# Optimization experiments

Measured on AMD Instinct MI355X. Metric: run time of the kernel, lower is better.

The kernel has to match this reference:

```python
import jax, jax.numpy as jnp
import numpy as np

B, D, H, L, E, NL, P, IMG, NT = 32, 768, 8, 6, 8, 256, 16, 224, 10
G = IMG // P          # 14 patches per side
NP = G * G            # 196 patches
HD = D // H           # 96 head dim
TOPK = 2
KEEP = 0.25
EPS = 1e-5


def layer_norm(x, g, b):
    m = x.mean(-1, keepdims=True)
    v = ((x - m) ** 2).mean(-1, keepdims=True)
    return (x - m) / jnp.sqrt(v + EPS) * g + b


def mha(q, kv, in_w, in_b, out_w, out_b):
    # torch nn.MultiheadAttention: packed in_proj (3D, D), out_proj (D, D)
    wq, wk, wv = in_w[:D], in_w[D:2 * D], in_w[2 * D:]
    bq, bk, bv = in_b[:D], in_b[D:2 * D], in_b[2 * D:]

    def heads(x, w, b):
        y = x @ w.T + b                               # (B, S, D)
        return y.reshape(x.shape[0], x.shape[1], H, HD).transpose(0, 2, 1, 3)

    Q = heads(q, wq, bq)
    K = heads(kv, wk, bk)
    V = heads(kv, wv, bv)
    scores = jnp.einsum('bhqd,bhkd->bhqk', Q, K) / np.sqrt(HD).astype(np.float32)
    attn = jax.nn.softmax(scores, axis=-1)
    o = jnp.einsum('bhqk,bhkd->bhqd', attn, V)
    o = o.transpose(0, 2, 1, 3).reshape(q.shape[0], q.shape[1], D)
    return o @ out_w.T + out_b


def moe(x, rw, rb, w1, b1, w2, b2):
    # top-2 routing; renormalize the top-k weights with a second softmax
    Bq, S, _ = x.shape
    T = Bq * S
    xt = x.reshape(T, D)
    probs = jax.nn.softmax(xt @ rw.T + rb, axis=-1)       # (T, E)
    tw, ti = jax.lax.top_k(probs, TOPK)                   # (T, K)
    tw = jax.nn.softmax(tw, axis=-1)
    # combine weights per expert: (T, E), >0 only for the chosen experts
    combine = (jax.nn.one_hot(ti, E, dtype=x.dtype) * tw[..., None]).sum(axis=1)
    out = jnp.zeros_like(xt)
    for e in range(E):  # fixed small expert count
        h = jax.nn.gelu(xt @ w1[e].T + b1[e], approximate=False)
        out = out + (h @ w2[e].T + b2[e]) * combine[:, e:e + 1]
    return out.reshape(Bq, S, D)


def _forward(images, type_ids, mask_noise, conv_w, conv_b, pos_emb, type_emb,
             latents, ca_in_w, ca_in_b, ca_out_w, ca_out_b, ca_ln_g, ca_ln_b,
             sa_in_w, sa_in_b, sa_out_w, sa_out_b, ln1_g, ln1_b,
             router_w, router_b, e_w1, e_b1, e_w2, e_b2, ln2_g, ln2_b):
    b = images.shape[0]
    # non-overlapping conv patch embed == unfold + matmul
    xp = images.reshape(b, 3, G, P, G, P).transpose(0, 2, 4, 1, 3, 5)
    xp = xp.reshape(b, NP, 3 * P * P)
    patches = xp @ conv_w.reshape(D, -1).T + conv_b        # (B, NP, D)
    patches = patches + pos_emb + type_emb[type_ids][:, None, :]
    # random masking: keep n_visible patches chosen by argsort of noise
    n_visible = int(NP * KEEP)
    order = jnp.argsort(mask_noise, axis=1)
    visible_indices = order[:, :n_visible]
    masked_indices = order[:, n_visible:]
    visible = jnp.take_along_axis(patches, visible_indices[:, :, None], axis=1)
    # cross attention from latents to visible patches
    lat = jnp.broadcast_to(latents, (b, NL, D))
    lat = layer_norm(lat + mha(lat, visible, ca_in_w, ca_in_b, ca_out_w, ca_out_b),
                     ca_ln_g, ca_ln_b)
    for l in range(L):
        a = mha(lat, lat, sa_in_w[l], sa_in_b[l], sa_out_w[l], sa_out_b[l])
        lat = layer_norm(lat + a, ln1_g[l], ln1_b[l])
        m = moe(lat, router_w[l], router_b[l], e_w1[l], e_b1[l], e_w2[l], e_b2[l])
        lat = layer_norm(lat + m, ln2_g[l], ln2_b[l])
    return lat, visible_indices, masked_indices


def setup_inputs() -> dict:
    key = jax.random.key(0)
    ks = jax.random.split(key, 16)
    r = lambda k, shape, s=0.02: jax.random.normal(k, shape, dtype=jnp.float32) * s
    z = lambda shape: jnp.zeros(shape, jnp.float32)
    o = lambda shape: jnp.ones(shape, jnp.float32)
    inp = {}
    inp['images'] = jax.random.normal(ks[0], (B, 3, IMG, IMG), dtype=jnp.float32)
    inp['type_ids'] = jax.random.randint(ks[1], (B,), 0, NT)
    inp['mask_noise'] = jax.random.uniform(ks[2], (B, NP), dtype=jnp.float32)
    inp['conv_w'] = r(ks[3], (D, 3, P, P))
    inp['conv_b'] = z((D,))
    inp['pos_emb'] = r(ks[4], (1, NP, D), 1.0)
    inp['type_emb'] = r(ks[5], (NT, D), 1.0)
    inp['latents'] = r(ks[6], (NL, D), 1.0)
    inp['ca_in_w'] = r(ks[7], (3 * D, D)); inp['ca_in_b'] = z((3 * D,))
    inp['ca_out_w'] = r(ks[8], (D, D)); inp['ca_out_b'] = z((D,))
    inp['ca_ln_g'] = o((D,)); inp['ca_ln_b'] = z((D,))
    inp['sa_in_w'] = r(ks[9], (L, 3 * D, D)); inp['sa_in_b'] = z((L, 3 * D))
    inp['sa_out_w'] = r(ks[10], (L, D, D)); inp['sa_out_b'] = z((L, D))
    inp['ln1_g'] = o((L, D)); inp['ln1_b'] = z((L, D))
    inp['router_w'] = r(ks[11], (L, E, D)); inp['router_b'] = z((L, E))
    inp['e_w1'] = r(ks[12], (L, E, 2 * D, D)); inp['e_b1'] = z((L, E, 2 * D))
    inp['e_w2'] = r(ks[13], (L, E, D, 2 * D)); inp['e_b2'] = z((L, E, D))
    inp['ln2_g'] = o((L, D)); inp['ln2_b'] = z((L, D))
    return inp


def reference(images, type_ids, mask_noise, conv_w, conv_b, pos_emb, type_emb,
              latents, ca_in_w, ca_in_b, ca_out_w, ca_out_b, ca_ln_g, ca_ln_b,
              sa_in_w, sa_in_b, sa_out_w, sa_out_b, ln1_g, ln1_b,
              router_w, router_b, e_w1, e_b1, e_w2, e_b2, ln2_g, ln2_b):
    return _forward(images, type_ids, mask_noise, conv_w, conv_b, pos_emb,
                    type_emb, latents, ca_in_w, ca_in_b, ca_out_w, ca_out_b,
                    ca_ln_g, ca_ln_b, sa_in_w, sa_in_b, sa_out_w, sa_out_b,
                    ln1_g, ln1_b, router_w, router_b, e_w1, e_b1, e_w2, e_b2,
                    ln2_g, ln2_b)
```

## Files before the change

### kernel.cpp

```cpp
#include <hip/hip_runtime.h>

typedef unsigned short u16;
typedef unsigned int u32;
typedef __attribute__((ext_vector_type(8))) u16 u16x8;
typedef __attribute__((ext_vector_type(8))) __bf16 bf16x8;
typedef __attribute__((ext_vector_type(4))) float f32x4;

#define DEV static __device__ __forceinline__

DEV float b2f(u16 u){ unsigned int i = ((unsigned int)u)<<16; float f; __builtin_memcpy(&f,&i,4); return f; }
DEV u16 f2b(float f){ unsigned int x; __builtin_memcpy(&x,&f,4); x = x + 0x7fffu + ((x>>16)&1u); return (u16)(x>>16); }

DEV void gll16(const u16* g, u16* l){
    __builtin_amdgcn_global_load_lds(
        (const __attribute__((address_space(1))) u32*)(const void*)g,
        (__attribute__((address_space(3))) u32*)(void*)l, 16, 0, 0);
}

template<bool F32>
DEV u16x8 ld8(const void* base, long off){
    if constexpr (F32){
        const float* p = (const float*)base + off;
        float4 a = *(const float4*)p;
        float4 b = *(const float4*)(p+4);
        u16x8 r;
        r[0]=f2b(a.x); r[1]=f2b(a.y); r[2]=f2b(a.z); r[3]=f2b(a.w);
        r[4]=f2b(b.x); r[5]=f2b(b.y); r[6]=f2b(b.z); r[7]=f2b(b.w);
        return r;
    } else {
        return *(const u16x8*)((const u16*)base + off);
    }
}
template<bool F32>
DEV const void* vadd(const void* p, long elems){
    if constexpr (F32) return (const void*)((const float*)p + elems);
    else               return (const void*)((const u16*)p + elems);
}

#define LAT_ELEMS 6291456
#define NVIS 49
#define NMASK 147
#define T_TOK 8192
#define MOE_CAP 17408
#define MOE_HALF 8704
#define KOFF 6291456L
#define VOFF 12582912L

__global__ __launch_bounds__(256) void wconv(const float* __restrict__ src, u16* __restrict__ dst, long n)
{
    long i = ((long)blockIdx.x*256 + threadIdx.x)*8;
    if (i >= n) return;
    *(u16x8*)(dst + i) = ld8<true>(src, i);
}

__global__ __launch_bounds__(256) void argsort_k(const float* __restrict__ noise,
                                                 int* __restrict__ order,
                                                 float* __restrict__ dout)
{
    __shared__ float vals[196];
    __shared__ int ord[196];
    int b = blockIdx.x, tid = threadIdx.x;
    if (tid < 196) vals[tid] = noise[b*196 + tid];
    __syncthreads();
    if (tid < 196){
        float vi = vals[tid]; int rank = 0;
        for (int j=0;j<196;j++){ float vj = vals[j]; rank += (vj < vi) || (vj == vi && j < tid); }
        ord[rank] = tid;
    }
    __syncthreads();
    if (tid < 196){
        int v = ord[tid];
        order[b*196 + tid] = v;
        if (tid < NVIS) dout[LAT_ELEMS + b*NVIS + tid] = (float)v;
        else            dout[LAT_ELEMS + 32*NVIS + b*NMASK + (tid - NVIS)] = (float)v;
    }
}

__global__ __launch_bounds__(256) void patch_gather(const float* __restrict__ images,
                                                    const int* __restrict__ order,
                                                    u16* __restrict__ Ap)
{
    int i = blockIdx.x*256 + threadIdx.x;
    int t = i/48, kc = i - t*48;
    if (t >= 1664) return;
    if (t >= 1568){
        u16x8 z{};
        *(u16x8*)(Ap + (long)t*768 + kc*16)     = z;
        *(u16x8*)(Ap + (long)t*768 + kc*16 + 8) = z;
        return;
    }
    int b = t/49, vi = t - b*49;
    int p = order[b*196 + vi];
    int c = kc >> 4, py = kc & 15;
    int gy = p/14, gx = p - gy*14;
    const float* src = images + (((long)(b*3 + c)*224 + gy*16 + py)*224 + gx*16);
    u16x8 o0 = ld8<true>(src, 0);
    u16x8 o1 = ld8<true>(src, 8);
    *(u16x8*)(Ap + (long)t*768 + kc*16)     = o0;
    *(u16x8*)(Ap + (long)t*768 + kc*16 + 8) = o1;
}

__global__ __launch_bounds__(256) void add_pos_type(u16* __restrict__ vis,
                                                    const int* __restrict__ order,
                                                    const int* __restrict__ type_ids,
                                                    const float* __restrict__ pos,
                                                    const float* __restrict__ temb)
{
    int i = blockIdx.x*256 + threadIdx.x;
    int t = i/96, dc = (i - t*96)*8;
    if (t >= 1568) return;
    int b = t/49, vi = t - b*49;
    int p = order[b*196 + vi], tb = type_ids[b];
    u16x8 a = *(u16x8*)(vis + (long)t*768 + dc);
    const float* pp = pos  + (long)p*768 + dc;
    const float* tt = temb + (long)tb*768 + dc;
    float4 p0 = *(const float4*)pp, p1 = *(const float4*)(pp+4);
    float4 t0 = *(const float4*)tt, t1 = *(const float4*)(tt+4);
    u16x8 o;
    o[0]=f2b(b2f(a[0])+p0.x+t0.x); o[1]=f2b(b2f(a[1])+p0.y+t0.y);
    o[2]=f2b(b2f(a[2])+p0.z+t0.z); o[3]=f2b(b2f(a[3])+p0.w+t0.w);
    o[4]=f2b(b2f(a[4])+p1.x+t1.x); o[5]=f2b(b2f(a[5])+p1.y+t1.y);
    o[6]=f2b(b2f(a[6])+p1.z+t1.z); o[7]=f2b(b2f(a[7])+p1.w+t1.w);
    *(u16x8*)(vis + (long)t*768 + dc) = o;
}

template<int BK, bool BIAS, bool GELU, int GRP, bool AF32, bool BF32, bool SWZ, bool GLL>
__global__ __launch_bounds__(256,2) void gemm_nt(
    const void* __restrict__ A, const void* __restrict__ B, const float* __restrict__ bias,
    u16* __restrict__ C,
    int M, int N, int K, int lda, int ldb, int ldc,
    float scale, int ZLO, int NB,
    long sAh, long sAl, long sBh, long sBl, long sCh, long sCl,
    const int* __restrict__ aoff, const int* __restrict__ tos, const u16* __restrict__ zbuf,
    int row_base, long sBE, long sBiasE)
{
    int bx = blockIdx.x, by = blockIdx.y;
    if (SWZ){
        int nx = gridDim.x, ny = gridDim.y;
        int nwg = nx*ny;
        int flat = by*nx + bx;
        int q = nwg >> 3, r = nwg & 7;
        int xcd = flat & 7, idx = flat >> 3;
        int wg = (xcd < r ? xcd*(q+1) : r*(q+1) + (xcd - r)*q) + idx;
        bx = wg % nx; by = wg / nx;
    }
    int z = blockIdx.z; int zh = z / ZLO, zl = z - zh*ZLO;
    const void* Ab = vadd<AF32>(A, zh*sAh + zl*sAl);
    const void* Bb = vadd<BF32>(B, zh*sBh + zl*sBl);
    u16* Cb = C + zh*sCh + zl*sCl;
    const float* biasb = bias;
    int row0 = by*128, col0 = bx*128;
    int lim = 0;
    if (GRP == 1 || GRP == 2){
        lim = aoff[8];
        int g0 = row_base + row0;
        if (g0 >= lim) return;
        int e = 0;
        #pragma unroll
        for (int i=1;i<8;i++) if (g0 >= aoff[i]) e = i;
        Bb = vadd<BF32>(B, (long)e*sBE);
        if (BIAS) biasb = bias + (long)e*sBiasE;
    }
    constexpr int SP = GLL ? BK : BK + 8;
    __shared__ __align__(16) u16 As[128*SP];
    __shared__ __align__(16) u16 Bs[128*SP];
    int tid = threadIdx.x;
    int lane = tid & 63, wv = tid >> 6;
    int wr = (wv>>1)*64, wc = (wv&1)*64;
    f32x4 acc[4][4];
    #pragma unroll
    for (int m=0;m<4;m++){
        #pragma unroll
        for (int n=0;n<4;n++) acc[m][n] = f32x4{0.f,0.f,0.f,0.f};
    }
    constexpr int RPC = BK/8;
    constexpr int PER = 128*RPC/256;
    int tA[4];
    if (GRP == 1){
        if (GLL){
            #pragma unroll
            for (int j=0;j<4;j++){
                int r = wv*32 + j*8 + (lane>>3);
                tA[j] = tos[row_base + row0 + r];
            }
        } else {
            #pragma unroll
            for (int j=0;j<PER && j<4;j++){
                int c = j*256 + tid;
                tA[j] = tos[row_base + row0 + c/RPC];
            }
        }
    }
    for (int k0=0; k0<K; k0+=BK){
        if constexpr (GLL){
            #pragma unroll
            for (int j=0;j<4;j++){
                int r  = wv*32 + j*8 + (lane>>3);
                int ch = lane & 7;
                const u16* sa;
                if (GRP == 1){
                    int t = tA[j];
                    sa = (t >= 0) ? (const u16*)Ab + (long)t*lda + k0 + ch*8 : zbuf + ch*8;
                } else {
                    sa = (const u16*)Ab + (long)(row0+r)*lda + k0 + ch*8;
                }
                gll16(sa, As + (wv*256 + j*64)*8);
                const u16* sb = (const u16*)Bb + (long)(col0+r)*ldb + k0 + ch*8;
                gll16(sb, Bs + (wv*256 + j*64)*8);
            }
        } else {
            #pragma unroll
            for (int j=0;j<PER;j++){
                int c = j*256 + tid;
                int r = c / RPC, cc = (c - r*RPC)*8;
                u16x8 va{}, vb{};
                if (GRP == 1){
                    int t = tA[j];
                    if (t >= 0) va = ld8<AF32>(Ab, (long)t*lda + k0 + cc);
                } else {
                    va = ld8<AF32>(Ab, (long)(row0+r)*lda + k0 + cc);
                }
                if (col0 + r < NB) vb = ld8<BF32>(Bb, (long)(col0+r)*ldb + k0 + cc);
                *(u16x8*)(As + r*SP + cc) = va;
                *(u16x8*)(Bs + r*SP + cc) = vb;
            }
        }
        __syncthreads();
        #pragma unroll
        for (int kk=0; kk<BK/32; kk++){
            bf16x8 af[4], bg[4];
            #pragma unroll
            for (int m=0;m<4;m++)
                af[m] = *(const bf16x8*)(As + (wr + m*16 + (lane&15))*SP + kk*32 + (lane>>4)*8);
            #pragma unroll
            for (int n=0;n<4;n++)
                bg[n] = *(const bf16x8*)(Bs + (wc + n*16 + (lane&15))*SP + kk*32 + (lane>>4)*8);
            #pragma unroll
            for (int m=0;m<4;m++){
                #pragma unroll
                for (int n=0;n<4;n++)
                    acc[m][n] = __builtin_amdgcn_mfma_f32_16x16x32_bf16(af[m], bg[n], acc[m][n], 0,0,0);
            }
        }
        __syncthreads();
    }
    #pragma unroll
    for (int m=0;m<4;m++){
        int rbase = row0 + wr + m*16 + ((lane>>4)<<2);
        #pragma unroll
        for (int n=0;n<4;n++){
            int col = col0 + wc + n*16 + (lane&15);
            if (col < N){
                float bv = BIAS ? biasb[col] : 0.f;
                #pragma unroll
                for (int j=0;j<4;j++){
                    int row = rbase + j;
                    bool ok = (row < M);
                    if (GRP == 1 || GRP == 2) ok = ok && (row_base + row) < lim;
                    if (ok){
                        float v = acc[m][n][j]*scale + bv;
                        if (GELU) v = 0.5f*v*(1.f + erff(v*0.70710678118f));
                        u16 ov = f2b(v);
                        if (GRP == 3){
                            if (col < 768){
                                Cb[(long)row*768 + col] = ov;
                            } else if (col < 1536){
                                Cb[sBE + (long)row*768 + (col - 768)] = ov;
                            } else {
                                int c96 = col - 1536;
                                int h = c96/96, d = c96 - h*96;
                                Cb[sBiasE + ((long)((row>>8)*8 + h)*96 + d)*256 + (row & 255)] = ov;
                            }
                        } else if (GRP == 2){
                            Cb[(long)(row_base + row)*ldc + col] = ov;
                        } else {
                            Cb[(long)row*ldc + col] = ov;
                        }
                    }
                }
            }
        }
    }
}

__global__ __launch_bounds__(256) void ca_attn(const u16* __restrict__ Qc,
                                               const u16* __restrict__ KV,
                                               u16* __restrict__ attn_out)
{
    __shared__ float Sm[256*49];
    __shared__ u16 KVs[49*96];
    int b = blockIdx.x, h = blockIdx.y, q = threadIdx.x;
    for (int i=q; i<49*96; i+=256){ int k=i/96, d=i-k*96; KVs[i] = KV[(long)(b*49+k)*1536 + h*96 + d]; }
    __syncthreads();
    float qv[96];
    #pragma unroll
    for (int d=0;d<96;d++) qv[d] = b2f(Qc[(long)q*768 + h*96 + d]);
    for (int k=0;k<49;k++){
        float a = 0.f;
        #pragma unroll
        for (int d=0;d<96;d++) a += qv[d]*b2f(KVs[k*96+d]);
        Sm[q*49+k] = a*0.10206207f;
    }
    __syncthreads();
    for (int i=q; i<49*96; i+=256){ int k=i/96, d=i-k*96; KVs[i] = KV[(long)(b*49+k)*1536 + 768 + h*96 + d]; }
    float mx = -1e30f;
    for (int k=0;k<49;k++) mx = fmaxf(mx, Sm[q*49+k]);
    float sum = 0.f;
    for (int k=0;k<49;k++){ float e = __expf(Sm[q*49+k]-mx); Sm[q*49+k]=e; sum+=e; }
    float inv = 1.f/sum;
    __syncthreads();
    for (int d=0;d<96;d++){
        float a = 0.f;
        for (int k=0;k<49;k++) a += Sm[q*49+k]*b2f(KVs[k*96+d]);
        attn_out[(long)(b*256+q)*768 + h*96 + d] = f2b(a*inv);
    }
}

__global__ __launch_bounds__(256) void softmax256(u16* __restrict__ S, int rows)
{
    int wid = threadIdx.x >> 6, lane = threadIdx.x & 63;
    int r = blockIdx.x*4 + wid; if (r >= rows) return;
    u16* p = S + (long)r*256;
    ushort4 v = *(const ushort4*)(p + lane*4);
    float x0=b2f(v.x), x1=b2f(v.y), x2=b2f(v.z), x3=b2f(v.w);
    float mx = fmaxf(fmaxf(x0,x1), fmaxf(x2,x3));
    #pragma unroll
    for (int off=32; off>=1; off>>=1) mx = fmaxf(mx, __shfl_xor(mx, off, 64));
    x0=__expf(x0-mx); x1=__expf(x1-mx); x2=__expf(x2-mx); x3=__expf(x3-mx);
    float s = x0+x1+x2+x3;
    #pragma unroll
    for (int off=32; off>=1; off>>=1) s += __shfl_xor(s, off, 64);
    float inv = 1.f/s;
    ushort4 o; o.x=f2b(x0*inv); o.y=f2b(x1*inv); o.z=f2b(x2*inv); o.w=f2b(x3*inv);
    *(ushort4*)(p + lane*4) = o;
}

template<int MODE>
__global__ __launch_bounds__(256) void ln_k(
    const float* __restrict__ res, int resmod,
    const u16* __restrict__ add,
    const u16* __restrict__ OutE, const int* __restrict__ sot, const float2* __restrict__ w01,
    const float* __restrict__ g, const float* __restrict__ bb,
    float* __restrict__ out, u16* __restrict__ outb, int T)
{
    int wid = threadIdx.x >> 6, lane = threadIdx.x & 63;
    int t = blockIdx.x*4 + wid; if (t >= T) return;
    const float* rp = res + (long)(t % resmod)*768;
    float x[12];
    #pragma unroll
    for (int j=0;j<3;j++){
        float4 v = *(const float4*)(rp + j*256 + lane*4);
        x[j*4+0]=v.x; x[j*4+1]=v.y; x[j*4+2]=v.z; x[j*4+3]=v.w;
    }
    if (MODE == 0){
        const u16* ap = add + (long)t*768;
        #pragma unroll
        for (int j=0;j<3;j++){
            ushort4 v = *(const ushort4*)(ap + j*256 + lane*4);
            x[j*4+0]+=b2f(v.x); x[j*4+1]+=b2f(v.y); x[j*4+2]+=b2f(v.z); x[j*4+3]+=b2f(v.w);
        }
    } else {
        int s0 = sot[2*t], s1 = sot[2*t+1];
        float2 w = w01[t];
        const u16* p0 = OutE + (long)s0*768;
        const u16* p1 = OutE + (long)s1*768;
        #pragma unroll
        for (int j=0;j<3;j++){
            ushort4 v0 = *(const ushort4*)(p0 + j*256 + lane*4);
            ushort4 v1 = *(const ushort4*)(p1 + j*256 + lane*4);
            x[j*4+0] += w.x*b2f(v0.x) + w.y*b2f(v1.x);
            x[j*4+1] += w.x*b2f(v0.y) + w.y*b2f(v1.y);
            x[j*4+2] += w.x*b2f(v0.z) + w.y*b2f(v1.z);
            x[j*4+3] += w.x*b2f(v0.w) + w.y*b2f(v1.w);
        }
    }
    float s = 0.f;
    #pragma unroll
    for (int i=0;i<12;i++) s += x[i];
    #pragma unroll
    for (int off=32; off>=1; off>>=1) s += __shfl_xor(s, off, 64);
    float m = s*(1.f/768.f);
    float s2 = 0.f;
    #pragma unroll
    for (int i=0;i<12;i++){ float d = x[i]-m; s2 += d*d; }
    #pragma unroll
    for (int off=32; off>=1; off>>=1) s2 += __shfl_xor(s2, off, 64);
    float rstd = rsqrtf(s2*(1.f/768.f) + 1e-5f);
    #pragma unroll
    for (int j=0;j<3;j++){
        int col = j*256 + lane*4;
        float4 gg = *(const float4*)(g + col);
        float4 bv = *(const float4*)(bb + col);
        float4 o;
        o.x = (x[j*4+0]-m)*rstd*gg.x + bv.x;
        o.y = (x[j*4+1]-m)*rstd*gg.y + bv.y;
        o.z = (x[j*4+2]-m)*rstd*gg.z + bv.z;
        o.w = (x[j*4+3]-m)*rstd*gg.w + bv.w;
        *(float4*)(out + (long)t*768 + col) = o;
        if (outb != nullptr){
            ushort4 ob;
            ob.x = f2b(o.x); ob.y = f2b(o.y); ob.z = f2b(o.z); ob.w = f2b(o.w);
            *(ushort4*)(outb + (long)t*768 + col) = ob;
        }
    }
}

__global__ __launch_bounds__(256) void router_k(const float* __restrict__ lat,
                                                const float* __restrict__ rw, const float* __restrict__ rb,
                                                int2* __restrict__ e01, float2* __restrict__ w01)
{
    int wid = threadIdx.x >> 6, lane = threadIdx.x & 63;
    int t = blockIdx.x*4 + wid; if (t >= T_TOK) return;
    const float* lp = lat + (long)t*768;
    float4 x[3];
    #pragma unroll
    for (int j=0;j<3;j++) x[j] = *(const float4*)(lp + j*256 + lane*4);
    float part[8];
    #pragma unroll
    for (int e=0;e<8;e++){
        const float* wp = rw + e*768;
        float a = 0.f;
        #pragma unroll
        for (int j=0;j<3;j++){
            float4 w4 = *(const float4*)(wp + j*256 + lane*4);
            a += x[j].x*w4.x + x[j].y*w4.y + x[j].z*w4.z + x[j].w*w4.w;
        }
        part[e] = a;
    }
    #pragma unroll
    for (int e=0;e<8;e++){
        #pragma unroll
        for (int off=32; off>=1; off>>=1) part[e] += __shfl_xor(part[e], off, 64);
    }
    if (lane == 0){
        float pe[8];
        float mx = -1e30f;
        #pragma unroll
        for (int e=0;e<8;e++){ pe[e] = part[e] + rb[e]; mx = fmaxf(mx, pe[e]); }
        float sum = 0.f;
        #pragma unroll
        for (int e=0;e<8;e++){ pe[e] = __expf(pe[e]-mx); sum += pe[e]; }
        float inv = 1.f/sum;
        #pragma unroll
        for (int e=0;e<8;e++) pe[e] *= inv;
        int i0 = 0;
        #pragma unroll
        for (int e=1;e<8;e++) if (pe[e] > pe[i0]) i0 = e;
        int i1 = -1;
        for (int e=0;e<8;e++){ if (e == i0) continue; if (i1 < 0 || pe[e] > pe[i1]) i1 = e; }
        float ex = __expf(pe[i1] - pe[i0]);
        float w0 = 1.f/(1.f+ex), w1 = ex/(1.f+ex);
        e01[t] = int2{i0, i1};
        w01[t] = float2{w0, w1};
    }
}

__global__ __launch_bounds__(256) void route_build(const int2* __restrict__ e01,
                                                   int* __restrict__ aoff_g,
                                                   int* __restrict__ tos, int* __restrict__ sot,
                                                   u16* __restrict__ zbuf)
{
    __shared__ int wsum[8][4];
    __shared__ int wbase[8][4];
    __shared__ int aoff_s[9];
    int tid = threadIdx.x, lane = tid & 63, wid = tid >> 6;
    for (int s = tid; s < MOE_CAP; s += 256) tos[s] = -1;
    if (tid < 128) zbuf[tid] = 0;
    int t0 = tid * 32;
    int lc[8];
    #pragma unroll
    for (int e=0;e<8;e++) lc[e] = 0;
    for (int i=0;i<32;i++){
        int2 e = e01[t0+i];
        lc[e.x]++; lc[e.y]++;
    }
    int excl[8];
    #pragma unroll
    for (int e=0;e<8;e++){
        int sc = lc[e];
        #pragma unroll
        for (int off=1; off<64; off<<=1){
            int n = __shfl_up(sc, off, 64);
            if (lane >= off) sc += n;
        }
        excl[e] = sc - lc[e];
        if (lane == 63) wsum[e][wid] = sc;
    }
    __syncthreads();
    if (tid == 0){
        int tot = 0;
        #pragma unroll
        for (int e=0;e<8;e++){
            int s = 0;
            #pragma unroll
            for (int w=0;w<4;w++){ wbase[e][w] = s; s += wsum[e][w]; }
            aoff_s[e] = tot;
            tot += (s + 127) & ~127;
        }
        aoff_s[8] = tot;
        #pragma unroll
        for (int e=0;e<9;e++) aoff_g[e] = aoff_s[e];
    }
    __syncthreads();
    int cur[8];
    #pragma unroll
    for (int e=0;e<8;e++) cur[e] = aoff_s[e] + wbase[e][wid] + excl[e];
    for (int i=0;i<32;i++){
        int t = t0 + i;
        int2 e = e01[t];
        int s0 = cur[e.x]++;
        tos[s0] = t; sot[2*t]   = s0;
        int s1 = cur[e.y]++;
        tos[s1] = t; sot[2*t+1] = s1;
    }
}

extern "C" void kernel_launch(void* const* d_in, const int* in_sizes, int n_in,
                              void* d_out, int out_size, void* d_ws, size_t ws_size,
                              hipStream_t stream)
{
    (void)in_sizes; (void)n_in; (void)out_size;
    const float* images   = (const float*)d_in[0];
    const int*   type_ids = (const int*)d_in[1];
    const float* noise    = (const float*)d_in[2];
    const float* conv_w   = (const float*)d_in[3];
    const float* conv_b   = (const float*)d_in[4];
    const float* pos_emb  = (const float*)d_in[5];
    const float* type_emb = (const float*)d_in[6];
    const float* latents  = (const float*)d_in[7];
    const float* ca_in_w  = (const float*)d_in[8];
    const float* ca_in_b  = (const float*)d_in[9];
    const float* ca_out_w = (const float*)d_in[10];
    const float* ca_out_b = (const float*)d_in[11];
    const float* ca_ln_g  = (const float*)d_in[12];
    const float* ca_ln_b  = (const float*)d_in[13];
    const float* sa_in_w  = (const float*)d_in[14];
    const float* sa_in_b  = (const float*)d_in[15];
    const float* sa_out_w = (const float*)d_in[16];
    const float* sa_out_b = (const float*)d_in[17];
    const float* ln1_g    = (const float*)d_in[18];
    const float* ln1_b    = (const float*)d_in[19];
    const float* router_w = (const float*)d_in[20];
    const float* router_b = (const float*)d_in[21];
    const float* e_w1     = (const float*)d_in[22];
    const float* e_b1     = (const float*)d_in[23];
    const float* e_w2     = (const float*)d_in[24];
    const float* e_b2     = (const float*)d_in[25];
    const float* ln2_g    = (const float*)d_in[26];
    const float* ln2_b    = (const float*)d_in[27];
    float* dout = (float*)d_out;
    float* lat  = dout;

    char* p = (char*)d_ws;
    auto alloc = [&](size_t n)->char*{ char* r = p; p += (n + 255) & ~(size_t)255; return r; };
    int*    order  = (int*)   alloc(32*196*4);
    int2*   e01    = (int2*)  alloc((size_t)T_TOK*8);
    float2* w01    = (float2*)alloc((size_t)T_TOK*8);
    int*    aoff   = (int*)   alloc(64);
    int*    tos    = (int*)   alloc((size_t)MOE_CAP*4);
    int*    sot    = (int*)   alloc((size_t)T_TOK*2*4);
    u16*    zbuf   = (u16*)   alloc(256);
    size_t aux_used = (size_t)(p - (char*)d_ws);
    bool wb  = ws_size >= aux_used + 92798976ull + 42467328ull;
    bool big = wb || ws_size >= aux_used + 92798976ull;
    u16* ar = (u16*)alloc(wb ? 135266304ull : (big ? 92798976ull : 71303168ull));
    u16* latb   = big ? ar : nullptr;
    u16* common = big ? ar + 6291456 : ar;
    u16* wbuf   = wb ? ar + 6291456 + 40108032 : nullptr;
    u16* Ap  = common;
    u16* vis = common + 1277952;
    u16* KV  = common + 2555904;
    u16* Qc  = common + 5111808;
    u16* caO = common + 5308416;
    u16* caM = common + 11599872;
    u16* Qb  = common;
    u16* Vt  = common + VOFF;
    u16* S   = common + 18874368;
    u16* aO  = common;
    u16* mha = common + KOFF;
    u16* Hbuf = common;
    u16* OutE = common + (big ? 26738688 : 13369344);
    u16* cwb   = wbuf;
    u16* cainb = wbuf + 589824;
    u16* caoutb= wbuf + 2359296;
    u16* winb  = wbuf;
    u16* woutb = wbuf + 1769472;
    u16* w1b   = wbuf + 2359296;
    u16* w2b   = wbuf + 11796480;

    const float ONE = 1.0f;
    const float SCL = 0.10206207f;
    const long Z0 = 0;

    argsort_k<<<32, 256, 0, stream>>>(noise, order, dout);
    patch_gather<<<312, 256, 0, stream>>>(images, order, Ap);
    if (wb){
        wconv<<<288, 256, 0, stream>>>(conv_w, cwb, 589824);
        wconv<<<864, 256, 0, stream>>>(ca_in_w, cainb, 1769472);
        wconv<<<288, 256, 0, stream>>>(ca_out_w, caoutb, 589824);
        gemm_nt<64,true,false,0,false,false,true,true><<<dim3(6,13,1),256,0,stream>>>(Ap, cwb, conv_b, vis,
            1664,768,768, 768,768,768, ONE, 1, 768, Z0,Z0,Z0,Z0,Z0,Z0, nullptr,nullptr,nullptr,0, Z0,Z0);
        add_pos_type<<<588, 256, 0, stream>>>(vis, order, type_ids, pos_emb, type_emb);
        gemm_nt<64,true,false,0,true,false,true,false><<<dim3(6,2,1),256,0,stream>>>(latents, cainb, ca_in_b, Qc,
            256,768,768, 768,768,768, ONE, 1, 768, Z0,Z0,Z0,Z0,Z0,Z0, nullptr,nullptr,nullptr,0, Z0,Z0);
        gemm_nt<64,true,false,0,false,false,true,true><<<dim3(12,13,1),256,0,stream>>>(vis, cainb + 589824, ca_in_b + 768, KV,
            1664,1536,768, 768,768,1536, ONE, 1, 1536, Z0,Z0,Z0,Z0,Z0,Z0, nullptr,nullptr,nullptr,0, Z0,Z0);
        ca_attn<<<dim3(32,8), 256, 0, stream>>>(Qc, KV, caO);
        gemm_nt<64,true,false,0,false,false,true,true><<<dim3(6,64,1),256,0,stream>>>(caO, caoutb, ca_out_b, caM,
            T_TOK,768,768, 768,768,768, ONE, 1, 768, Z0,Z0,Z0,Z0,Z0,Z0, nullptr,nullptr,nullptr,0, Z0,Z0);
    } else {
        gemm_nt<64,true,false,0,false,true,false,false><<<dim3(6,13,1),256,0,stream>>>(Ap, conv_w, conv_b, vis,
            1664,768,768, 768,768,768, ONE, 1, 768, Z0,Z0,Z0,Z0,Z0,Z0, nullptr,nullptr,nullptr,0, Z0,Z0);
        add_pos_type<<<588, 256, 0, stream>>>(vis, order, type_ids, pos_emb, type_emb);
        gemm_nt<64,true,false,0,true,true,false,false><<<dim3(6,2,1),256,0,stream>>>(latents, ca_in_w, ca_in_b, Qc,
            256,768,768, 768,768,768, ONE, 1, 768, Z0,Z0,Z0,Z0,Z0,Z0, nullptr,nullptr,nullptr,0, Z0,Z0);
        gemm_nt<64,true,false,0,false,true,false,false><<<dim3(12,13,1),256,0,stream>>>(vis, ca_in_w + 768*768, ca_in_b + 768, KV,
            1664,1536,768, 768,768,1536, ONE, 1, 1536, Z0,Z0,Z0,Z0,Z0,Z0, nullptr,nullptr,nullptr,0, Z0,Z0);
        ca_attn<<<dim3(32,8), 256, 0, stream>>>(Qc, KV, caO);
        gemm_nt<64,true,false,0,false,true,false,false><<<dim3(6,64,1),256,0,stream>>>(caO, ca_out_w, ca_out_b, caM,
            T_TOK,768,768, 768,768,768, ONE, 1, 768, Z0,Z0,Z0,Z0,Z0,Z0, nullptr,nullptr,nullptr,0, Z0,Z0);
    }
    ln_k<0><<<2048, 256, 0, stream>>>(latents, 256, caM, nullptr,nullptr,nullptr, ca_ln_g, ca_ln_b, lat, latb, T_TOK);

    for (int l=0; l<6; l++){
        const float* w_in  = sa_in_w  + (long)l*2304*768;
        const float* b_in  = sa_in_b  + l*2304;
        const float* w_out = sa_out_w + (long)l*768*768;
        const float* b_out = sa_out_b + l*768;
        const float* w1 = e_w1 + (long)l*8*1536*768;
        const float* b1 = e_b1 + l*8*1536;
        const float* w2 = e_w2 + (long)l*8*768*1536;
        const float* b2 = e_b2 + l*8*768;
        if (wb){
            wconv<<<864, 256, 0, stream>>>(w_in, winb, 1769472);
            wconv<<<288, 256, 0, stream>>>(w_out, woutb, 589824);
            wconv<<<4608, 256, 0, stream>>>(w1, w1b, 9437184);
            wconv<<<4608, 256, 0, stream>>>(w2, w2b, 9437184);
            gemm_nt<64,true,false,3,false,false,true,true><<<dim3(18,64,1),256,0,stream>>>(latb, winb, b_in, Qb,
                T_TOK,2304,768, 768,768,0, ONE, 1, 2304, Z0,Z0,Z0,Z0,Z0,Z0, nullptr,nullptr,nullptr,0, KOFF, VOFF);
        } else if (big){
            gemm_nt<64,true,false,3,false,true,false,false><<<dim3(18,64,1),256,0,stream>>>(latb, w_in, b_in, Qb,
                T_TOK,2304,768, 768,768,0, ONE, 1, 2304, Z0,Z0,Z0,Z0,Z0,Z0, nullptr,nullptr,nullptr,0, KOFF, VOFF);
        } else {
            gemm_nt<64,true,false,3,true,true,false,false><<<dim3(18,64,1),256,0,stream>>>(lat, w_in, b_in, Qb,
                T_TOK,2304,768, 768,768,0, ONE, 1, 2304, Z0,Z0,Z0,Z0,Z0,Z0, nullptr,nullptr,nullptr,0, KOFF, VOFF);
        }
        gemm_nt<32,false,false,0,false,false,false,false><<<dim3(2,2,256),256,0,stream>>>(Qb, Qb + KOFF, nullptr, S,
            256,256,96, 768,768,256, SCL, 8, 256, 196608,96, 196608,96, 524288,65536, nullptr,nullptr,nullptr,0, Z0,Z0);
        softmax256<<<16384, 256, 0, stream>>>(S, 65536);
        gemm_nt<64,false,false,0,false,false,false,false><<<dim3(1,2,256),256,0,stream>>>(S, Vt, nullptr, aO,
            256,96,256, 256,256,768, ONE, 8, 96, 524288,65536, 196608,24576, 196608,96, nullptr,nullptr,nullptr,0, Z0,Z0);
        if (wb){
            gemm_nt<64,true,false,0,false,false,true,true><<<dim3(6,64,1),256,0,stream>>>(aO, woutb, b_out, mha,
                T_TOK,768,768, 768,768,768, ONE, 1, 768, Z0,Z0,Z0,Z0,Z0,Z0, nullptr,nullptr,nullptr,0, Z0,Z0);
        } else {
            gemm_nt<64,true,false,0,false,true,false,false><<<dim3(6,64,1),256,0,stream>>>(aO, w_out, b_out, mha,
                T_TOK,768,768, 768,768,768, ONE, 1, 768, Z0,Z0,Z0,Z0,Z0,Z0, nullptr,nullptr,nullptr,0, Z0,Z0);
        }
        ln_k<0><<<2048, 256, 0, stream>>>(lat, T_TOK, mha, nullptr,nullptr,nullptr, ln1_g + l*768, ln1_b + l*768, lat, latb, T_TOK);
        router_k<<<2048, 256, 0, stream>>>(lat, router_w + l*8*768, router_b + l*8, e01, w01);
        route_build<<<1, 256, 0, stream>>>(e01, aoff, tos, sot, zbuf);
        if (wb){
            gemm_nt<64,true,true,1,false,false,true,true><<<dim3(12,136,1),256,0,stream>>>(latb, w1b, b1, Hbuf,
                MOE_CAP,1536,768, 768,768,1536, ONE, 1, 1536, Z0,Z0,Z0,Z0,Z0,Z0,
                aoff, tos, zbuf, 0, (long)1536*768, 1536);
            gemm_nt<64,true,false,2,false,false,true,true><<<dim3(6,136,1),256,0,stream>>>(Hbuf, w2b, b2, OutE,
                MOE_CAP,768,1536, 1536,1536,768, ONE, 1, 768, Z0,Z0,Z0,Z0,Z0,Z0,
                aoff, tos, zbuf, 0, (long)768*1536, 768);
        } else if (big){
            gemm_nt<64,true,true,1,false,true,false,false><<<dim3(12,136,1),256,0,stream>>>(latb, w1, b1, Hbuf,
                MOE_CAP,1536,768, 768,768,1536, ONE, 1, 1536, Z0,Z0,Z0,Z0,Z0,Z0,
                aoff, tos, zbuf, 0, (long)1536*768, 1536);
            gemm_nt<64,true,false,2,false,true,false,false><<<dim3(6,136,1),256,0,stream>>>(Hbuf, w2, b2, OutE,
                MOE_CAP,768,1536, 1536,1536,768, ONE, 1, 768, Z0,Z0,Z0,Z0,Z0,Z0,
                aoff, tos, zbuf, 0, (long)768*1536, 768);
        } else {
            for (int rb2=0; rb2<MOE_CAP; rb2+=MOE_HALF){
                gemm_nt<64,true,true,1,true,true,false,false><<<dim3(12,68,1),256,0,stream>>>(lat, w1, b1, Hbuf,
                    MOE_HALF,1536,768, 768,768,1536, ONE, 1, 1536, Z0,Z0,Z0,Z0,Z0,Z0,
                    aoff, tos, zbuf, rb2, (long)1536*768, 1536);
                gemm_nt<64,true,false,2,false,true,false,false><<<dim3(6,68,1),256,0,stream>>>(Hbuf, w2, b2, OutE,
                    MOE_HALF,768,1536, 1536,1536,768, ONE, 1, 768, Z0,Z0,Z0,Z0,Z0,Z0,
                    aoff, tos, zbuf, rb2, (long)768*1536, 768);
            }
        }
        ln_k<1><<<2048, 256, 0, stream>>>(lat, T_TOK, nullptr, OutE, sot, w01, ln2_g + l*768, ln2_b + l*768, lat, latb, T_TOK);
    }
}
```

Before: 2.744 ms.

## Hoist all per-layer weight conversions upfront and generalize async LDS loads

```diff
diff --git a/kernel.cpp b/kernel.cpp
--- a/kernel.cpp
+++ b/kernel.cpp
@@ -125,7 +125,7 @@
 }
 
 template<int BK, bool BIAS, bool GELU, int GRP, bool AF32, bool BF32, bool SWZ, bool GLL>
-__global__ __launch_bounds__(256,2) void gemm_nt(
+__global__ __launch_bounds__(256,4) void gemm_nt(
     const void* __restrict__ A, const void* __restrict__ B, const float* __restrict__ bias,
     u16* __restrict__ C,
     int M, int N, int K, int lda, int ldb, int ldc,
@@ -174,13 +174,15 @@
         for (int n=0;n<4;n++) acc[m][n] = f32x4{0.f,0.f,0.f,0.f};
     }
     constexpr int RPC = BK/8;
+    constexpr int RPI = 64/RPC;
+    constexpr int NJ  = 32/RPI;
     constexpr int PER = 128*RPC/256;
     int tA[4];
     if (GRP == 1){
         if (GLL){
             #pragma unroll
-            for (int j=0;j<4;j++){
-                int r = wv*32 + j*8 + (lane>>3);
+            for (int j=0;j<NJ;j++){
+                int r = wv*32 + j*RPI + (lane/RPC);
                 tA[j] = tos[row_base + row0 + r];
             }
         } else {
@@ -194,9 +196,9 @@
     for (int k0=0; k0<K; k0+=BK){
         if constexpr (GLL){
             #pragma unroll
-            for (int j=0;j<4;j++){
-                int r  = wv*32 + j*8 + (lane>>3);
-                int ch = lane & 7;
+            for (int j=0;j<NJ;j++){
+                int r  = wv*32 + j*RPI + (lane/RPC);
+                int ch = lane % RPC;
                 const u16* sa;
                 if (GRP == 1){
                     int t = tA[j];
@@ -204,9 +206,10 @@
                 } else {
                     sa = (const u16*)Ab + (long)(row0+r)*lda + k0 + ch*8;
                 }
-                gll16(sa, As + (wv*256 + j*64)*8);
-                const u16* sb = (const u16*)Bb + (long)(col0+r)*ldb + k0 + ch*8;
-                gll16(sb, Bs + (wv*256 + j*64)*8);
+                gll16(sa, As + (wv*32 + j*RPI)*BK);
+                const u16* sb = (col0 + r < NB) ? (const u16*)Bb + (long)(col0+r)*ldb + k0 + ch*8
+                                                : zbuf + ch*8;
+                gll16(sb, Bs + (wv*32 + j*RPI)*BK);
             }
         } else {
             #pragma unroll
@@ -561,12 +564,13 @@
     int*    sot    = (int*)   alloc((size_t)T_TOK*2*4);
     u16*    zbuf   = (u16*)   alloc(256);
     size_t aux_used = (size_t)(p - (char*)d_ws);
-    bool wb  = ws_size >= aux_used + 92798976ull + 42467328ull;
+    const size_t WB_BYTES = 92798976ull + 260702208ull;
+    bool wb  = ws_size >= aux_used + WB_BYTES;
     bool big = wb || ws_size >= aux_used + 92798976ull;
-    u16* ar = (u16*)alloc(wb ? 135266304ull : (big ? 92798976ull : 71303168ull));
+    u16* ar = (u16*)alloc(wb ? WB_BYTES : (big ? 92798976ull : 71303168ull));
     u16* latb   = big ? ar : nullptr;
     u16* common = big ? ar + 6291456 : ar;
-    u16* wbuf   = wb ? ar + 6291456 + 40108032 : nullptr;
+    u16* wbufA  = wb ? ar + 6291456 + 40108032 : nullptr;
     u16* Ap  = common;
     u16* vis = common + 1277952;
     u16* KV  = common + 2555904;
@@ -580,13 +584,13 @@
     u16* mha = common + KOFF;
     u16* Hbuf = common;
     u16* OutE = common + (big ? 26738688 : 13369344);
-    u16* cwb   = wbuf;
-    u16* cainb = wbuf + 589824;
-    u16* caoutb= wbuf + 2359296;
-    u16* winb  = wbuf;
-    u16* woutb = wbuf + 1769472;
-    u16* w1b   = wbuf + 2359296;
-    u16* w2b   = wbuf + 11796480;
+    u16* cwb      = wbufA;
+    u16* cainb    = wbufA + 589824;
+    u16* caoutb   = wbufA + 2359296;
+    u16* winbAll  = wbufA + 2949120;
+    u16* woutbAll = wbufA + 13565952;
+    u16* w1bAll   = wbufA + 17104896;
+    u16* w2bAll   = wbufA + 73728000;
 
     const float ONE = 1.0f;
     const float SCL = 0.10206207f;
@@ -598,92 +602,103 @@
         wconv<<<288, 256, 0, stream>>>(conv_w, cwb, 589824);
         wconv<<<864, 256, 0, stream>>>(ca_in_w, cainb, 1769472);
         wconv<<<288, 256, 0, stream>>>(ca_out_w, caoutb, 589824);
+        wconv<<<5184, 256, 0, stream>>>(sa_in_w, winbAll, 10616832);
+        wconv<<<1728, 256, 0, stream>>>(sa_out_w, woutbAll, 3538944);
+        wconv<<<27648, 256, 0, stream>>>(e_w1, w1bAll, 56623104);
+        wconv<<<27648, 256, 0, stream>>>(e_w2, w2bAll, 56623104);
         gemm_nt<64,true,false,0,false,false,true,true><<<dim3(6,13,1),256,0,stream>>>(Ap, cwb, conv_b, vis,
-            1664,768,768, 768,768,768, ONE, 1, 768, Z0,Z0,Z0,Z0,Z0,Z0, nullptr,nullptr,nullptr,0, Z0,Z0);
+            1664,768,768, 768,768,768, ONE, 1, 768, Z0,Z0,Z0,Z0,Z0,Z0, nullptr,nullptr,zbuf,0, Z0,Z0);
         add_pos_type<<<588, 256, 0, stream>>>(vis, order, type_ids, pos_emb, type_emb);
         gemm_nt<64,true,false,0,true,false,true,false><<<dim3(6,2,1),256,0,stream>>>(latents, cainb, ca_in_b, Qc,
-            256,768,768, 768,768,768, ONE, 1, 768, Z0,Z0,Z0,Z0,Z0,Z0, nullptr,nullptr,nullptr,0, Z0,Z0);
+            256,768,768, 768,768,768, ONE, 1, 768, Z0,Z0,Z0,Z0,Z0,Z0, nullptr,nullptr,zbuf,0, Z0,Z0);
         gemm_nt<64,true,false,0,false,false,true,true><<<dim3(12,13,1),256,0,stream>>>(vis, cainb + 589824, ca_in_b + 768, KV,
-            1664,1536,768, 768,768,1536, ONE, 1, 1536, Z0,Z0,Z0,Z0,Z0,Z0, nullptr,nullptr,nullptr,0, Z0,Z0);
+            1664,1536,768, 768,768,1536, ONE, 1, 1536, Z0,Z0,Z0,Z0,Z0,Z0, nullptr,nullptr,zbuf,0, Z0,Z0);
         ca_attn<<<dim3(32,8), 256, 0, stream>>>(Qc, KV, caO);
         gemm_nt<64,true,false,0,false,false,true,true><<<dim3(6,64,1),256,0,stream>>>(caO, caoutb, ca_out_b, caM,
-            T_TOK,768,768, 768,768,768, ONE, 1, 768, Z0,Z0,Z0,Z0,Z0,Z0, nullptr,nullptr,nullptr,0, Z0,Z0);
+            T_TOK,768,768, 768,768,768, ONE, 1, 768, Z0,Z0,Z0,Z0,Z0,Z0, nullptr,nullptr,zbuf,0, Z0,Z0);
     } else {
         gemm_nt<64,true,false,0,false,true,false,false><<<dim3(6,13,1),256,0,stream>>>(Ap, conv_w, conv_b, vis,
-            1664,768,768, 768,768,768, ONE, 1, 768, Z0,Z0,Z0,Z0,Z0,Z0, nullptr,nullptr,nullptr,0, Z0,Z0);
+            1664,768,768, 768,768,768, ONE, 1, 768, Z0,Z0,Z0,Z0,Z0,Z0, nullptr,nullptr,zbuf,0, Z0,Z0);
         add_pos_type<<<588, 256, 0, stream>>>(vis, order, type_ids, pos_emb, type_emb);
         gemm_nt<64,true,false,0,true,true,false,false><<<dim3(6,2,1),256,0,stream>>>(latents, ca_in_w, ca_in_b, Qc,
-            256,768,768, 768,768,768, ONE, 1, 768, Z0,Z0,Z0,Z0,Z0,Z0, nullptr,nullptr,nullptr,0, Z0,Z0);
+            256,768,768, 768,768,768, ONE, 1, 768, Z0,Z0,Z0,Z0,Z0,Z0, nullptr,nullptr,zbuf,0, Z0,Z0);
         gemm_nt<64,true,false,0,false,true,false,false><<<dim3(12,13,1),256,0,stream>>>(vis, ca_in_w + 768*768, ca_in_b + 768, KV,
-            1664,1536,768, 768,768,1536, ONE, 1, 1536, Z0,Z0,Z0,Z0,Z0,Z0, nullptr,nullptr,nullptr,0, Z0,Z0);
+            1664,1536,768, 768,768,1536, ONE, 1, 1536, Z0,Z0,Z0,Z0,Z0,Z0, nullptr,nullptr,zbuf,0, Z0,Z0);
         ca_attn<<<dim3(32,8), 256, 0, stream>>>(Qc, KV, caO);
         gemm_nt<64,true,false,0,false,true,false,false><<<dim3(6,64,1),256,0,stream>>>(caO, ca_out_w, ca_out_b, caM,
-            T_TOK,768,768, 768,768,768, ONE, 1, 768, Z0,Z0,Z0,Z0,Z0,Z0, nullptr,nullptr,nullptr,0, Z0,Z0);
+            T_TOK,768,768, 768,768,768, ONE, 1, 768, Z0,Z0,Z0,Z0,Z0,Z0, nullptr,nullptr,zbuf,0, Z0,Z0);
     }
     ln_k<0><<<2048, 256, 0, stream>>>(latents, 256, caM, nullptr,nullptr,nullptr, ca_ln_g, ca_ln_b, lat, latb, T_TOK);
 
     for (int l=0; l<6; l++){
-        const float* w_in  = sa_in_w  + (long)l*2304*768;
         const float* b_in  = sa_in_b  + l*2304;
-        const float* w_out = sa_out_w + (long)l*768*768;
         const float* b_out = sa_out_b + l*768;
-        const float* w1 = e_w1 + (long)l*8*1536*768;
         const float* b1 = e_b1 + l*8*1536;
-        const float* w2 = e_w2 + (long)l*8*768*1536;
         const float* b2 = e_b2 + l*8*768;
         if (wb){
-            wconv<<<864, 256, 0, stream>>>(w_in, winb, 1769472);
-            wconv<<<288, 256, 0, stream>>>(w_out, woutb, 589824);
-            wconv<<<4608, 256, 0, stream>>>(w1, w1b, 9437184);
-            wconv<<<4608, 256, 0, stream>>>(w2, w2b, 9437184);
+            const u16* winb  = winbAll  + (long)l*1769472;
+            const u16* woutb = woutbAll + (long)l*589824;
+            const u16* w1b   = w1bAll   + (long)l*9437184;
+            const u16* w2b   = w2bAll   + (long)l*9437184;
             gemm_nt<64,true,false,3,false,false,true,true><<<dim3(18,64,1),256,0,stream>>>(latb, winb, b_in, Qb,
-                T_TOK,2304,768, 768,768,0, ONE, 1, 2304, Z0,Z0,Z0,Z0,Z0,Z0, nullptr,nullptr,nullptr,0, KOFF, VOFF);
-        } else if (big){
-            gemm_nt<64,true,false,3,false,true,false,false><<<dim3(18,64,1),256,0,stream>>>(latb, w_in, b_in, Qb,
-                T_TOK,2304,768, 768,768,0, ONE, 1, 2304, Z0,Z0,Z0,Z0,Z0,Z0, nullptr,nullptr,nullptr,0, KOFF, VOFF);
-        } else {
-            gemm_nt<64,true,false,3,true,true,false,false><<<dim3(18,64,1),256,0,stream>>>(lat, w_in, b_in, Qb,
-                T_TOK,2304,768, 768,768,0, ONE, 1, 2304, Z0,Z0,Z0,Z0,Z0,Z0, nullptr,nullptr,nullptr,0, KOFF, VOFF);
-        }
-        gemm_nt<32,false,false,0,false,false,false,false><<<dim3(2,2,256),256,0,stream>>>(Qb, Qb + KOFF, nullptr, S,
-            256,256,96, 768,768,256, SCL, 8, 256, 196608,96, 196608,96, 524288,65536, nullptr,nullptr,nullptr,0, Z0,Z0);
-        softmax256<<<16384, 256, 0, stream>>>(S, 65536);
-        gemm_nt<64,false,false,0,false,false,false,false><<<dim3(1,2,256),256,0,stream>>>(S, Vt, nullptr, aO,
-            256,96,256, 256,256,768, ONE, 8, 96, 524288,65536, 196608,24576, 196608,96, nullptr,nullptr,nullptr,0, Z0,Z0);
-        if (wb){
+                T_TOK,2304,768, 768,768,0, ONE, 1, 2304, Z0,Z0,Z0,Z0,Z0,Z0, nullptr,nullptr,zbuf,0, KOFF, VOFF);
+            gemm_nt<32,false,false,0,false,false,false,true><<<dim3(2,2,256),256,0,stream>>>(Qb, Qb + KOFF, nullptr, S,
+                256,256,96, 768,768,256, SCL, 8, 256, 196608,96, 196608,96, 524288,65536, nullptr,nullptr,zbuf,0, Z0,Z0);
+            softmax256<<<16384, 256, 0, stream>>>(S, 65536);
+            gemm_nt<64,false,false,0,false,false,false,true><<<dim3(1,2,256),256,0,stream>>>(S, Vt, nullptr, aO,
+                256,96,256, 256,256,768, ONE, 8, 96, 524288,65536, 196608,24576, 196608,96, nullptr,nullptr,zbuf,0, Z0,Z0);
             gemm_nt<64,true,false,0,false,false,true,true><<<dim3(6,64,1),256,0,stream>>>(aO, woutb, b_out, mha,
-                T_TOK,768,768, 768,768,768, ONE, 1, 768, Z0,Z0,Z0,Z0,Z0,Z0, nullptr,nullptr,nullptr,0, Z0,Z0);
-        } else {
-            gemm_nt<64,true,false,0,false,true,false,false><<<dim3(6,64,1),256,0,stream>>>(aO, w_out, b_out, mha,
-                T_TOK,768,768, 768,768,768, ONE, 1, 768, Z0,Z0,Z0,Z0,Z0,Z0, nullptr,nullptr,nullptr,0, Z0,Z0);
-        }
-        ln_k<0><<<2048, 256, 0, stream>>>(lat, T_TOK, mha, nullptr,nullptr,nullptr, ln1_g + l*768, ln1_b + l*768, lat, latb, T_TOK);
-        router_k<<<2048, 256, 0, stream>>>(lat, router_w + l*8*768, router_b + l*8, e01, w01);
-        route_build<<<1, 256, 0, stream>>>(e01, aoff, tos, sot, zbuf);
-        if (wb){
+                T_TOK,768,768, 768,768,768, ONE, 1, 768, Z0,Z0,Z0,Z0,Z0,Z0, nullptr,nullptr,zbuf,0, Z0,Z0);
+            ln_k<0><<<2048, 256, 0, stream>>>(lat, T_TOK, mha, nullptr,nullptr,nullptr, ln1_g + l*768, ln1_b + l*768, lat, latb, T_TOK);
+            router_k<<<2048, 256, 0, stream>>>(lat, router_w + l*8*768, router_b + l*8, e01, w01);
+            route_build<<<1, 256, 0, stream>>>(e01, aoff, tos, sot, zbuf);
             gemm_nt<64,true,true,1,false,false,true,true><<<dim3(12,136,1),256,0,stream>>>(latb, w1b, b1, Hbuf,
                 MOE_CAP,1536,768, 768,768,1536, ONE, 1, 1536, Z0,Z0,Z0,Z0,Z0,Z0,
                 aoff, tos, zbuf, 0, (long)1536*768, 1536);
             gemm_nt<64,true,false,2,false,false,true,true><<<dim3(6,136,1),256,0,stream>>>(Hbuf, w2b, b2, OutE,
                 MOE_CAP,768,1536, 1536,1536,768, ONE, 1, 768, Z0,Z0,Z0,Z0,Z0,Z0,
                 aoff, tos, zbuf, 0, (long)768*1536, 768);
-        } else if (big){
-            gemm_nt<64,true,true,1,false,true,false,false><<<dim3(12,136,1),256,0,stream>>>(latb, w1, b1, Hbuf,
-                MOE_CAP,1536,768, 768,768,1536, ONE, 1, 1536, Z0,Z0,Z0,Z0,Z0,Z0,
-                aoff, tos, zbuf, 0, (long)1536*768, 1536);
-            gemm_nt<64,true,false,2,false,true,false,false><<<dim3(6,136,1),256,0,stream>>>(Hbuf, w2, b2, OutE,
-                MOE_CAP,768,1536, 1536,1536,768, ONE, 1, 768, Z0,Z0,Z0,Z0,Z0,Z0,
-                aoff, tos, zbuf, 0, (long)768*1536, 768);
+            ln_k<1><<<2048, 256, 0, stream>>>(lat, T_TOK, nullptr, OutE, sot, w01, ln2_g + l*768, ln2_b + l*768, lat, latb, T_TOK);
         } else {
-            for (int rb2=0; rb2<MOE_CAP; rb2+=MOE_HALF){
-                gemm_nt<64,true,true,1,true,true,false,false><<<dim3(12,68,1),256,0,stream>>>(lat, w1, b1, Hbuf,
-                    MOE_HALF,1536,768, 768,768,1536, ONE, 1, 1536, Z0,Z0,Z0,Z0,Z0,Z0,
-                    aoff, tos, zbuf, rb2, (long)1536*768, 1536);
-                gemm_nt<64,true,false,2,false,true,false,false><<<dim3(6,68,1),256,0,stream>>>(Hbuf, w2, b2, OutE,
-                    MOE_HALF,768,1536, 1536,1536,768, ONE, 1, 768, Z0,Z0,Z0,Z0,Z0,Z0,
-                    aoff, tos, zbuf, rb2, (long)768*1536, 768);
+            const float* w_in  = sa_in_w  + (long)l*2304*768;
+            const float* w_out = sa_out_w + (long)l*768*768;
+            const float* w1 = e_w1 + (long)l*8*1536*768;
+            const float* w2 = e_w2 + (long)l*8*768*1536;
+            if (big){
+                gemm_nt<64,true,false,3,false,true,false,false><<<dim3(18,64,1),256,0,stream>>>(latb, w_in, b_in, Qb,
+                    T_TOK,2304,768, 768,768,0, ONE, 1, 2304, Z0,Z0,Z0,Z0,Z0,Z0, nullptr,nullptr,zbuf,0, KOFF, VOFF);
+            } else {
+                gemm_nt<64,true,false,3,true,true,false,false><<<dim3(18,64,1),256,0,stream>>>(lat, w_in, b_in, Qb,
+                    T_TOK,2304,768, 768,768,0, ONE, 1, 2304, Z0,Z0,Z0,Z0,Z0,Z0, nullptr,nullptr,zbuf,0, KOFF, VOFF);
             }
-        }
-        ln_k<1><<<2048, 256, 0, stream>>>(lat, T_TOK, nullptr, OutE, sot, w01, ln2_g + l*768, ln2_b + l*768, lat, latb, T_TOK);
-    }
-}
+            gemm_nt<32,false,false,0,false,false,false,false><<<dim3(2,2,256),256,0,stream>>>(Qb, Qb + KOFF, nullptr, S,
+                256,256,96, 768,768,256, SCL, 8, 256, 196608,96, 196608,96, 524288,65536, nullptr,nullptr,zbuf,0, Z0,Z0);
+            softmax256<<<16384, 256, 0, stream>>>(S, 65536);
+            gemm_nt<64,false,false,0,false,false,false,false><<<dim3(1,2,256),256,0,stream>>>(S, Vt, nullptr, aO,
+                256,96,256, 256,256,768, ONE, 8, 96, 524288,65536, 196608,24576, 196608,96, nullptr,nullptr,zbuf,0, Z0,Z0);
+            gemm_nt<64,true,false,0,false,true,false,false><<<dim3(6,64,1),256,0,stream>>>(aO, w_out, b_out, mha,
+                T_TOK,768,768, 768,768,768, ONE, 1, 768, Z0,Z0,Z0,Z0,Z0,Z0, nullptr,nullptr,zbuf,0, Z0,Z0);
+            ln_k<0><<<2048, 256, 0, stream>>>(lat, T_TOK, mha, nullptr,nullptr,nullptr, ln1_g + l*768, ln1_b + l*768, lat, latb, T_TOK);
+            router_k<<<2048, 256, 0, stream>>>(lat, router_w + l*8*768, router_b + l*8, e01, w01);
+            route_build<<<1, 256, 0, stream>>>(e01, aoff, tos, sot, zbuf);
+            if (big){
+                gemm_nt<64,true,true,1,false,true,false,false><<<dim3(12,136,1),256,0,stream>>>(latb, w1, b1, Hbuf,
+                    MOE_CAP,1536,768, 768,768,1536, ONE, 1, 1536, Z0,Z0,Z0,Z0,Z0,Z0,
+                    aoff, tos, zbuf, 0, (long)1536*768, 1536);
+                gemm_nt<64,true,false,2,false,true,false,false><<<dim3(6,136,1),256,0,stream>>>(Hbuf, w2, b2, OutE,
+                    MOE_CAP,768,1536, 1536,1536,768, ONE, 1, 768, Z0,Z0,Z0,Z0,Z0,Z0,
+                    aoff, tos, zbuf, 0, (long)768*1536, 768);
+            } else {
+                for (int rb2=0; rb2<MOE_CAP; rb2+=MOE_HALF){
+                    gemm_nt<64,true,true,1,true,true,false,false><<<dim3(12,68,1),256,0,stream>>>(lat, w1, b1, Hbuf,
+                        MOE_HALF,1536,768, 768,768,1536, ONE, 1, 1536, Z0,Z0,Z0,Z0,Z0,Z0,
+                        aoff, tos, zbuf, rb2, (long)1536*768, 1536);
+                    gemm_nt<64,true,false,2,false,true,false,false><<<dim3(6,68,1),256,0,stream>>>(Hbuf, w2, b2, OutE,
+                        MOE_HALF,768,1536, 1536,1536,768, ONE, 1, 768, Z0,Z0,Z0,Z0,Z0,Z0,
+                        aoff, tos, zbuf, rb2, (long)768*1536, 768);
+                }
+            }
+            ln_k<1><<<2048, 256, 0, stream>>>(lat, T_TOK, nullptr, OutE, sot, w01, ln2_g + l*768, ln2_b + l*768, lat, latb, T_TOK);
+        }
+    }
+}
```

After: 2.528 ms. 1.09x faster.
